# Optimization experiments

Measured on AMD Instinct MI355X. Metric: run time of the kernel, lower is better.

## Reference

```python
import jax, jax.numpy as jnp
import numpy as np

DIM = 512
NUM_HEADS = 8
HEAD_SIZE = 64
INNER = NUM_HEADS * HEAD_SIZE  # 512


def setup_inputs() -> dict:
    key = jax.random.key(0)
    k1, k2, k3, k4, k5 = jax.random.split(key, 5)
    x = jax.random.normal(k1, (2, 4096, DIM), dtype=jnp.float32)
    # Linear params stored as [in, out] for y = x @ W + b (same math as torch Linear)
    w_qkv = jax.random.normal(k2, (DIM, INNER * 3), dtype=jnp.float32) * (1.0 / np.sqrt(DIM))
    b_qkv = jax.random.normal(k3, (INNER * 3,), dtype=jnp.float32) * 0.01
    w_out = jax.random.normal(k4, (INNER, DIM), dtype=jnp.float32) * (1.0 / np.sqrt(INNER))
    b_out = jax.random.normal(k5, (DIM,), dtype=jnp.float32) * 0.01
    return {"x": x, "w_qkv": w_qkv, "b_qkv": b_qkv, "w_out": w_out, "b_out": b_out}


def reference(x, w_qkv, b_qkv, w_out, b_out):
    b, n, _ = x.shape
    qkv = x @ w_qkv + b_qkv                      # [b, n, 3*inner]
    q, k, v = jnp.split(qkv, 3, axis=-1)          # each [b, n, inner]

    def heads(t):  # 'b n (h d) -> b h n d'
        return t.reshape(b, n, NUM_HEADS, HEAD_SIZE).transpose(0, 2, 1, 3)

    q, k, v = heads(q), heads(k), heads(v)
    scores = jnp.einsum('bhnd,bhmd->bhnm', q, k) / jnp.sqrt(jnp.float32(HEAD_SIZE))
    probs = jax.nn.softmax(scores, axis=-1)       # dropout is identity in eval
    out = jnp.einsum('bhnm,bhmd->bhnd', probs, v)
    out = out.transpose(0, 2, 1, 3).reshape(b, n, INNER)  # 'b h n d -> b n (h d)'
    return out @ w_out + b_out
```

## Files before the change

### kernel.cpp

```cpp
#include <hip/hip_runtime.h>

typedef __bf16 bf16;
typedef __bf16 bf16x8 __attribute__((ext_vector_type(8)));
typedef float f32x4 __attribute__((ext_vector_type(4)));
typedef unsigned u32x4 __attribute__((ext_vector_type(4)));

#define MFMA16(a, b, c) __builtin_amdgcn_mfma_f32_16x16x32_bf16((a), (b), (c), 0, 0, 0)

static __device__ __forceinline__ bf16x8 ldg8(const bf16* p) {
  return *(const bf16x8*)p;
}
static __device__ __forceinline__ unsigned cvt_pk_bf16(float lo, float hi) {
  unsigned d;
  asm("v_cvt_pk_bf16_f32 %0, %1, %2" : "=v"(d) : "v"(lo), "v"(hi));
  return d;
}
static __device__ __forceinline__ void pl32_swap(unsigned& a, unsigned& b) {
  asm("v_permlane32_swap_b32 %0, %1" : "+v"(a), "+v"(b));
}
static __device__ __forceinline__ void pl16_swap(unsigned& a, unsigned& b) {
  asm("v_permlane16_swap_b32 %0, %1" : "+v"(a), "+v"(b));
}


__global__ __launch_bounds__(256) void pack_weights(const float* __restrict__ Wqkv,
                                                    const float* __restrict__ Wout,
                                                    bf16* __restrict__ Wp1,
                                                    bf16* __restrict__ Wp2) {
  __shared__ float tile[32 * 129];
  int kc = blockIdx.x, nt = blockIdx.y;
  const float* W;
  bf16* dst;
  int N, ntl;
  if (nt < 12) {
    W = Wqkv; N = 1536; ntl = nt;
    dst = Wp1 + ((size_t)ntl * 16 + kc) * 4096;
  } else {
    W = Wout; N = 512; ntl = nt - 12;
    dst = Wp2 + ((size_t)ntl * 16 + kc) * 4096;
  }
  int row = threadIdx.x >> 3;
  int c0 = (threadIdx.x & 7) * 16;
  const float* src = W + (size_t)(kc * 32 + row) * N + ntl * 128 + c0;
#pragma unroll
  for (int i = 0; i < 4; i++) {
    float4 v = *(const float4*)(src + i * 4);
    tile[row * 129 + c0 + i * 4 + 0] = v.x;
    tile[row * 129 + c0 + i * 4 + 1] = v.y;
    tile[row * 129 + c0 + i * 4 + 2] = v.z;
    tile[row * 129 + c0 + i * 4 + 3] = v.w;
  }
  __syncthreads();
#pragma unroll
  for (int half = 0; half < 2; half++) {
    int U = threadIdx.x + half * 256;
    int kchunk = U >> 7, n = U & 127;
    bf16x8 o;
#pragma unroll
    for (int j = 0; j < 8; j++) o[j] = (bf16)tile[(kchunk * 8 + j) * 129 + n];
    *(bf16x8*)&dst[U * 8] = o;
  }
}

__global__ __launch_bounds__(256, 3) void qkv_gemm(const float* __restrict__ x,
                                                   const bf16* __restrict__ Wp1,
                                                   const float* __restrict__ bqkv,
                                                   bf16* __restrict__ Q,
                                                   bf16* __restrict__ Kh,
                                                   bf16* __restrict__ Vt) {
  int mt = blockIdx.x, nt = blockIdx.y;
  int tid = threadIdx.x;
  int wave = tid >> 6, lane = tid & 63;
  int l16 = lane & 15, quad = lane >> 4;
  int wr = wave >> 1, wc = wave & 1;

  __shared__ __align__(16) bf16 SM[16384];

  int r = tid >> 1, khalf = tid & 1;
  const float* xs = x + (size_t)(mt * 128 + r) * 512 + khalf * 16;
  const bf16* Bt = Wp1 + (size_t)nt * 16 * 4096;
  int lwA0 = ((khalf * 2 + 0) * 128 + r) * 8;
  int lwA1 = ((khalf * 2 + 1) * 128 + r) * 8;

  float4 fa0 = *(const float4*)(xs + 0);
  float4 fa1 = *(const float4*)(xs + 4);
  float4 fa2 = *(const float4*)(xs + 8);
  float4 fa3 = *(const float4*)(xs + 12);
  bf16x8 pb0 = ldg8(Bt + tid * 8), pb1 = ldg8(Bt + 2048 + tid * 8);

  f32x4 acc[4][4] = {};
#pragma unroll 2
  for (int kc = 0; kc < 16; kc++) {
    bf16* A = SM + (kc & 1) * 4096;
    bf16* B = SM + 8192 + (kc & 1) * 4096;
    bf16x8 a0, a1;
    a0[0] = (bf16)fa0.x; a0[1] = (bf16)fa0.y; a0[2] = (bf16)fa0.z; a0[3] = (bf16)fa0.w;
    a0[4] = (bf16)fa1.x; a0[5] = (bf16)fa1.y; a0[6] = (bf16)fa1.z; a0[7] = (bf16)fa1.w;
    a1[0] = (bf16)fa2.x; a1[1] = (bf16)fa2.y; a1[2] = (bf16)fa2.z; a1[3] = (bf16)fa2.w;
    a1[4] = (bf16)fa3.x; a1[5] = (bf16)fa3.y; a1[6] = (bf16)fa3.z; a1[7] = (bf16)fa3.w;
    *(bf16x8*)&A[lwA0] = a0;
    *(bf16x8*)&A[lwA1] = a1;
    *(bf16x8*)&B[tid * 8] = pb0;
    *(bf16x8*)&B[2048 + tid * 8] = pb1;
    __syncthreads();
    if (kc < 15) {
      const float* xn = xs + (kc + 1) * 32;
      fa0 = *(const float4*)(xn + 0);
      fa1 = *(const float4*)(xn + 4);
      fa2 = *(const float4*)(xn + 8);
      fa3 = *(const float4*)(xn + 12);
      const bf16* bn = Bt + (kc + 1) * 4096;
      pb0 = ldg8(bn + tid * 8);
      pb1 = ldg8(bn + 2048 + tid * 8);
    }
    bf16x8 af[4], bfr[4];
#pragma unroll
    for (int fi = 0; fi < 4; fi++)
      af[fi] = *(const bf16x8*)&A[(quad * 128 + wr * 64 + fi * 16 + l16) * 8];
#pragma unroll
    for (int fj = 0; fj < 4; fj++)
      bfr[fj] = *(const bf16x8*)&B[(quad * 128 + wc * 64 + fj * 16 + l16) * 8];
    __builtin_amdgcn_s_setprio(1);
#pragma unroll
    for (int fi = 0; fi < 4; fi++)
#pragma unroll
      for (int fj = 0; fj < 4; fj++)
        acc[fi][fj] = MFMA16(af[fi], bfr[fj], acc[fi][fj]);
    __builtin_amdgcn_s_setprio(0);
  }

  __syncthreads();
  const int TS = 72;
  int b = mt >> 5;

  if (nt < 8) {
    bool isQ = nt < 4;
    bf16* dstb = isQ ? Q : Kh;
    int hb = isQ ? nt * 2 : (nt - 4) * 2;
#pragma unroll
    for (int ph = 0; ph < 2; ph++) {
      if (wc == ph) {
#pragma unroll
        for (int fj = 0; fj < 4; fj++) {
          float bias = bqkv[nt * 128 + wc * 64 + fj * 16 + l16];
#pragma unroll
          for (int fi = 0; fi < 4; fi++)
#pragma unroll
            for (int rr = 0; rr < 4; rr++) {
              float v = acc[fi][fj][rr] + bias;
              if (isQ) v *= 0.18033688f;
              SM[(wr * 64 + fi * 16 + quad * 4 + rr) * TS + fj * 16 + l16] =
                  (bf16)v;
            }
        }
      }
      __syncthreads();
      int bh = b * 8 + hb + ph;
      bf16* dh = dstb + (size_t)bh * 4096 * 64 + (size_t)((mt & 31) * 128) * 64;
#pragma unroll
      for (int i = 0; i < 4; i++) {
        int U = tid + i * 256;
        int mr = U >> 3, oct = U & 7;
        bf16x8 v = ldg8(&SM[mr * TS + oct * 8]);
        *(bf16x8*)&dh[(size_t)mr * 64 + oct * 8] = v;
      }
      __syncthreads();
    }
  } else {
    int h0 = (nt - 8) * 2;
#pragma unroll
    for (int ph = 0; ph < 2; ph++) {
      if (wr == ph) {
#pragma unroll
        for (int fj = 0; fj < 4; fj++) {
          float bias = bqkv[nt * 128 + wc * 64 + fj * 16 + l16];
          int cp = wc * 64 + fj * 16 + l16;
#pragma unroll
          for (int fi = 0; fi < 4; fi++)
#pragma unroll
            for (int rr = 0; rr < 4; rr++)
              SM[cp * TS + fi * 16 + quad * 4 + rr] =
                  (bf16)(acc[fi][fj][rr] + bias);
        }
      }
      __syncthreads();
      int nb = (mt & 31) * 2 + ph;
#pragma unroll
      for (int i = 0; i < 4; i++) {
        int U = tid + i * 256;
        int cp = U >> 3, oct = U & 7;
        int h = h0 + (cp >> 6), d = cp & 63;
        int bh = b * 8 + h;
        bf16x8 v = ldg8(&SM[cp * TS + oct * 8]);
        *(bf16x8*)&Vt[(((size_t)bh * 64 + nb) * 64 + d) * 64 + oct * 8] = v;
      }
      __syncthreads();
    }
  }
}

__global__ __launch_bounds__(256, 4) void flash_partial(const bf16* __restrict__ Q,
                                                        const bf16* __restrict__ K,
                                                        const bf16* __restrict__ Vt,
                                                        bf16* __restrict__ Opart,
                                                        float* __restrict__ Lpart) {
  int strip = blockIdx.x, bh = blockIdx.y, qtr = blockIdx.z;
  int tid = threadIdx.x;
  int wave = tid >> 6, lane = tid & 63;
  int l16 = lane & 15, quad = lane >> 4;

  const bf16* Qh = Q + (size_t)bh * 4096 * 64;
  const bf16* Kg = K + ((size_t)bh * 4096 + qtr * 1024) * 64;
  const bf16* Vg = Vt + (size_t)bh * 64 * 4096 + (size_t)qtr * 1024 * 64;

  __shared__ __align__(16) bf16 Klds[2][4096];
  __shared__ __align__(16) bf16 Vlds[2][4096];

  int qbase = strip * 128 + wave * 32;
  bf16x8 aq[2][2];
#pragma unroll
  for (int mt = 0; mt < 2; mt++) {
    const bf16* qr = Qh + (size_t)(qbase + mt * 16 + l16) * 64;
    aq[mt][0] = ldg8(qr + quad * 8);
    aq[mt][1] = ldg8(qr + 32 + quad * 8);
  }

  bf16x8 ones;
#pragma unroll
  for (int i = 0; i < 8; i++) ones[i] = (bf16)1.0f;

  f32x4 o[2][4] = {};
  f32x4 acc_l[2] = {};

  int e0 = tid * 8, e1 = (256 + tid) * 8;
  int r0 = e0 >> 6, r1 = e1 >> 6;
  int u0 = r0 * 8 + (((e0 & 63) >> 3) ^ (r0 & 7));
  int u1 = r1 * 8 + (((e1 & 63) >> 3) ^ (r1 & 7));

  bf16x8 kp0 = ldg8(Kg + e0), kp1 = ldg8(Kg + e1);
  bf16x8 vp0 = ldg8(Vg + e0), vp1 = ldg8(Vg + e1);

#pragma unroll 2
  for (int t = 0; t < 16; t++) {
    int cur = t & 1;
    bf16* kl = Klds[cur];
    bf16* vl = Vlds[cur];
    *(bf16x8*)&kl[u0 * 8] = kp0;
    *(bf16x8*)&kl[u1 * 8] = kp1;
    *(bf16x8*)&vl[u0 * 8] = vp0;
    *(bf16x8*)&vl[u1 * 8] = vp1;
    __syncthreads();

    if (t < 15) {
      const bf16* kg = Kg + (size_t)(t + 1) * 4096;
      const bf16* vg = Vg + (size_t)(t + 1) * 4096;
      kp0 = ldg8(kg + e0);
      kp1 = ldg8(kg + e1);
      vp0 = ldg8(vg + e0);
      vp1 = ldg8(vg + e1);
    }

#pragma unroll
    for (int h2 = 0; h2 < 2; h2++) {
      f32x4 s[2][2] = {};
      __builtin_amdgcn_s_setprio(1);
#pragma unroll
      for (int c2 = 0; c2 < 2; c2++) {
        int n = h2 * 32 + c2 * 16 + l16;
        bf16x8 k0 = *(const bf16x8*)&kl[(n * 8 + (quad ^ (n & 7))) * 8];
        bf16x8 k1 = *(const bf16x8*)&kl[(n * 8 + ((4 + quad) ^ (n & 7))) * 8];
#pragma unroll
        for (int mt = 0; mt < 2; mt++) {
          s[mt][c2] = MFMA16(k0, aq[mt][0], s[mt][c2]);
          s[mt][c2] = MFMA16(k1, aq[mt][1], s[mt][c2]);
        }
      }
      __builtin_amdgcn_s_setprio(0);

      bf16x8 pa[2];
#pragma unroll
      for (int mt = 0; mt < 2; mt++) {
        unsigned ue[2], wo[2];
#pragma unroll
        for (int c2 = 0; c2 < 2; c2++) {
          float p0 = __builtin_amdgcn_exp2f(s[mt][c2][0]);
          float p1 = __builtin_amdgcn_exp2f(s[mt][c2][1]);
          float p2 = __builtin_amdgcn_exp2f(s[mt][c2][2]);
          float p3 = __builtin_amdgcn_exp2f(s[mt][c2][3]);
          ue[c2] = cvt_pk_bf16(p0, p1);
          wo[c2] = cvt_pk_bf16(p2, p3);
        }
        pl32_swap(ue[0], ue[1]);
        pl16_swap(ue[0], ue[1]);
        pl32_swap(wo[0], wo[1]);
        pl16_swap(wo[0], wo[1]);
        u32x4 pk = {ue[0], wo[0], ue[1], wo[1]};
        pa[mt] = __builtin_bit_cast(bf16x8, pk);
      }

      __builtin_amdgcn_s_setprio(1);
      acc_l[0] = MFMA16(pa[0], ones, acc_l[0]);
      acc_l[1] = MFMA16(pa[1], ones, acc_l[1]);
#pragma unroll
      for (int ct = 0; ct < 4; ct++) {
        int d = ct * 16 + l16;
        bf16x8 bv = *(const bf16x8*)&vl[(d * 8 + ((h2 * 4 + quad) ^ (d & 7))) * 8];
        o[0][ct] = MFMA16(pa[0], bv, o[0][ct]);
        o[1][ct] = MFMA16(pa[1], bv, o[1][ct]);
      }
      __builtin_amdgcn_s_setprio(0);
    }
  }

  size_t ub = ((size_t)qtr * 16 + bh) * 32 + strip;
  bf16* op = Opart + ub * 8192;
#pragma unroll
  for (int mt = 0; mt < 2; mt++) {
#pragma unroll
    for (int ct = 0; ct < 4; ct++)
#pragma unroll
      for (int r = 0; r < 4; r++)
        op[(wave * 32 + mt * 16 + quad * 4 + r) * 64 + ct * 16 + l16] =
            (bf16)o[mt][ct][r];
    if (l16 == 0) {
#pragma unroll
      for (int r = 0; r < 4; r++)
        Lpart[ub * 128 + wave * 32 + mt * 16 + quad * 4 + r] = acc_l[mt][r];
    }
  }
}

__global__ __launch_bounds__(256) void flash_combine(const bf16* __restrict__ Opart,
                                                     const float* __restrict__ Lpart,
                                                     bf16* __restrict__ Ap) {
  int mt = blockIdx.x, kc = blockIdx.y;
  int b = mt >> 5, strip = mt & 31;
  int h = kc >> 1, d0 = (kc & 1) * 32;
  int bh = b * 8 + h;
  size_t u[4];
#pragma unroll
  for (int q = 0; q < 4; q++) u[q] = ((size_t)q * 16 + bh) * 32 + strip;
  bf16* dst = Ap + ((size_t)mt * 16 + kc) * 4096;
#pragma unroll
  for (int hf = 0; hf < 2; hf++) {
    int U = threadIdx.x + hf * 256;
    int kchunk = U >> 7, r = U & 127;
    float acc[8] = {};
    float ls = 0.f;
#pragma unroll
    for (int q = 0; q < 4; q++) {
      bf16x8 ov = ldg8(&Opart[u[q] * 8192 + r * 64 + d0 + kchunk * 8]);
#pragma unroll
      for (int j = 0; j < 8; j++) acc[j] += (float)ov[j];
      ls += Lpart[u[q] * 128 + r];
    }
    float rl = 1.0f / ls;
    bf16x8 o;
#pragma unroll
    for (int j = 0; j < 8; j++) o[j] = (bf16)(acc[j] * rl);
    *(bf16x8*)&dst[U * 8] = o;
  }
}

__global__ __launch_bounds__(256, 3) void out_gemm(const bf16* __restrict__ Ap,
                                                   const bf16* __restrict__ Wp2,
                                                   const float* __restrict__ bout,
                                                   float* __restrict__ Out) {
  int mt = blockIdx.x, nt = blockIdx.y;
  int tid = threadIdx.x;
  int wave = tid >> 6, lane = tid & 63;
  int l16 = lane & 15, quad = lane >> 4;
  int wr = wave >> 1, wc = wave & 1;

  __shared__ __align__(16) bf16 SM[16384];

  const bf16* At = Ap + (size_t)mt * 16 * 4096;
  const bf16* Bt = Wp2 + (size_t)nt * 16 * 4096;
  bf16x8 pa0 = ldg8(At + tid * 8), pa1 = ldg8(At + 2048 + tid * 8);
  bf16x8 pb0 = ldg8(Bt + tid * 8), pb1 = ldg8(Bt + 2048 + tid * 8);

  f32x4 acc[4][4] = {};
#pragma unroll 2
  for (int kc = 0; kc < 16; kc++) {
    bf16* A = SM + (kc & 1) * 4096;
    bf16* B = SM + 8192 + (kc & 1) * 4096;
    *(bf16x8*)&A[tid * 8] = pa0;
    *(bf16x8*)&A[2048 + tid * 8] = pa1;
    *(bf16x8*)&B[tid * 8] = pb0;
    *(bf16x8*)&B[2048 + tid * 8] = pb1;
    __syncthreads();
    if (kc < 15) {
      const bf16* an = At + (kc + 1) * 4096;
      const bf16* bn = Bt + (kc + 1) * 4096;
      pa0 = ldg8(an + tid * 8);
      pa1 = ldg8(an + 2048 + tid * 8);
      pb0 = ldg8(bn + tid * 8);
      pb1 = ldg8(bn + 2048 + tid * 8);
    }
    bf16x8 af[4], bfr[4];
#pragma unroll
    for (int fi = 0; fi < 4; fi++)
      af[fi] = *(const bf16x8*)&A[(quad * 128 + wr * 64 + fi * 16 + l16) * 8];
#pragma unroll
    for (int fj = 0; fj < 4; fj++)
      bfr[fj] = *(const bf16x8*)&B[(quad * 128 + wc * 64 + fj * 16 + l16) * 8];
    __builtin_amdgcn_s_setprio(1);
#pragma unroll
    for (int fi = 0; fi < 4; fi++)
#pragma unroll
      for (int fj = 0; fj < 4; fj++)
        acc[fi][fj] = MFMA16(af[fi], bfr[fj], acc[fi][fj]);
    __builtin_amdgcn_s_setprio(0);
  }

#pragma unroll
  for (int fj = 0; fj < 4; fj++) {
    int c = nt * 128 + wc * 64 + fj * 16 + l16;
    float bias = bout[c];
#pragma unroll
    for (int fi = 0; fi < 4; fi++) {
#pragma unroll
      for (int r = 0; r < 4; r++) {
        int m = mt * 128 + wr * 64 + fi * 16 + quad * 4 + r;
        Out[(size_t)m * 512 + c] = acc[fi][fj][r] + bias;
      }
    }
  }
}

extern "C" void kernel_launch(void* const* d_in, const int* in_sizes, int n_in,
                              void* d_out, int out_size, void* d_ws,
                              size_t ws_size, hipStream_t stream) {
  const float* x = (const float*)d_in[0];
  const float* w_qkv = (const float*)d_in[1];
  const float* b_qkv = (const float*)d_in[2];
  const float* w_out = (const float*)d_in[3];
  const float* b_out = (const float*)d_in[4];
  float* out = (float*)d_out;

  char* ws = (char*)d_ws;
  bf16* Q = (bf16*)(ws + 0);
  bf16* K = (bf16*)(ws + 8388608);
  bf16* Vt = (bf16*)(ws + 16777216);
  bf16* Wp2 = (bf16*)(ws + 25165824);
  bf16* Opart = (bf16*)(ws + 25690112);
  float* Lpart = (float*)(ws + 59244544);
  bf16* Wp1 = (bf16*)(ws + 34078720);
  bf16* Ap = (bf16*)(ws + 0);

  pack_weights<<<dim3(16, 16), 256, 0, stream>>>(w_qkv, w_out, Wp1, Wp2);
  qkv_gemm<<<dim3(64, 12), 256, 0, stream>>>(x, Wp1, b_qkv, Q, K, Vt);
  flash_partial<<<dim3(32, 16, 4), 256, 0, stream>>>(Q, K, Vt, Opart, Lpart);
  flash_combine<<<dim3(64, 16), 256, 0, stream>>>(Opart, Lpart, Ap);
  out_gemm<<<dim3(64, 4), 256, 0, stream>>>(Ap, Wp2, b_out, out);
}
```

Baseline: 197.6 us.

## Halve flash KV split, load GEMM B from global, shrink out_gemm tiles

Flash attention now splits the KV sequence into 2 parts instead of 4. This halves the partial-output traffic and simplifies the combine kernel, but each block runs a longer loop. The QKV GEMM reads B fragments straight from global memory instead of staging them through LDS, and converts A with packed bf16 conversion instructions. out_gemm uses 64-row tiles with global B loads, doubling its grid for better occupancy at the cost of more redundant B reads.

```diff
diff --git a/kernel.cpp b/kernel.cpp
--- a/kernel.cpp
+++ b/kernel.cpp
@@ -74,7 +74,7 @@
   int l16 = lane & 15, quad = lane >> 4;
   int wr = wave >> 1, wc = wave & 1;
 
-  __shared__ __align__(16) bf16 SM[16384];
+  __shared__ __align__(16) bf16 SM[9216];
 
   int r = tid >> 1, khalf = tid & 1;
   const float* xs = x + (size_t)(mt * 128 + r) * 512 + khalf * 16;
@@ -86,22 +86,17 @@
   float4 fa1 = *(const float4*)(xs + 4);
   float4 fa2 = *(const float4*)(xs + 8);
   float4 fa3 = *(const float4*)(xs + 12);
-  bf16x8 pb0 = ldg8(Bt + tid * 8), pb1 = ldg8(Bt + 2048 + tid * 8);
 
   f32x4 acc[4][4] = {};
 #pragma unroll 2
   for (int kc = 0; kc < 16; kc++) {
     bf16* A = SM + (kc & 1) * 4096;
-    bf16* B = SM + 8192 + (kc & 1) * 4096;
-    bf16x8 a0, a1;
-    a0[0] = (bf16)fa0.x; a0[1] = (bf16)fa0.y; a0[2] = (bf16)fa0.z; a0[3] = (bf16)fa0.w;
-    a0[4] = (bf16)fa1.x; a0[5] = (bf16)fa1.y; a0[6] = (bf16)fa1.z; a0[7] = (bf16)fa1.w;
-    a1[0] = (bf16)fa2.x; a1[1] = (bf16)fa2.y; a1[2] = (bf16)fa2.z; a1[3] = (bf16)fa2.w;
-    a1[4] = (bf16)fa3.x; a1[5] = (bf16)fa3.y; a1[6] = (bf16)fa3.z; a1[7] = (bf16)fa3.w;
-    *(bf16x8*)&A[lwA0] = a0;
-    *(bf16x8*)&A[lwA1] = a1;
-    *(bf16x8*)&B[tid * 8] = pb0;
-    *(bf16x8*)&B[2048 + tid * 8] = pb1;
+    u32x4 pk0 = {cvt_pk_bf16(fa0.x, fa0.y), cvt_pk_bf16(fa0.z, fa0.w),
+                 cvt_pk_bf16(fa1.x, fa1.y), cvt_pk_bf16(fa1.z, fa1.w)};
+    u32x4 pk1 = {cvt_pk_bf16(fa2.x, fa2.y), cvt_pk_bf16(fa2.z, fa2.w),
+                 cvt_pk_bf16(fa3.x, fa3.y), cvt_pk_bf16(fa3.z, fa3.w)};
+    *(bf16x8*)&A[lwA0] = __builtin_bit_cast(bf16x8, pk0);
+    *(bf16x8*)&A[lwA1] = __builtin_bit_cast(bf16x8, pk1);
     __syncthreads();
     if (kc < 15) {
       const float* xn = xs + (kc + 1) * 32;
@@ -109,17 +104,15 @@
       fa1 = *(const float4*)(xn + 4);
       fa2 = *(const float4*)(xn + 8);
       fa3 = *(const float4*)(xn + 12);
-      const bf16* bn = Bt + (kc + 1) * 4096;
-      pb0 = ldg8(bn + tid * 8);
-      pb1 = ldg8(bn + 2048 + tid * 8);
     }
     bf16x8 af[4], bfr[4];
 #pragma unroll
     for (int fi = 0; fi < 4; fi++)
       af[fi] = *(const bf16x8*)&A[(quad * 128 + wr * 64 + fi * 16 + l16) * 8];
+    const bf16* Bk = Bt + kc * 4096;
 #pragma unroll
     for (int fj = 0; fj < 4; fj++)
-      bfr[fj] = *(const bf16x8*)&B[(quad * 128 + wc * 64 + fj * 16 + l16) * 8];
+      bfr[fj] = ldg8(Bk + (quad * 128 + wc * 64 + fj * 16 + l16) * 8);
     __builtin_amdgcn_s_setprio(1);
 #pragma unroll
     for (int fi = 0; fi < 4; fi++)
@@ -204,14 +197,14 @@
                                                         const bf16* __restrict__ Vt,
                                                         bf16* __restrict__ Opart,
                                                         float* __restrict__ Lpart) {
-  int strip = blockIdx.x, bh = blockIdx.y, qtr = blockIdx.z;
+  int strip = blockIdx.x, bh = blockIdx.y, half = blockIdx.z;
   int tid = threadIdx.x;
   int wave = tid >> 6, lane = tid & 63;
   int l16 = lane & 15, quad = lane >> 4;
 
   const bf16* Qh = Q + (size_t)bh * 4096 * 64;
-  const bf16* Kg = K + ((size_t)bh * 4096 + qtr * 1024) * 64;
-  const bf16* Vg = Vt + (size_t)bh * 64 * 4096 + (size_t)qtr * 1024 * 64;
+  const bf16* Kg = K + ((size_t)bh * 4096 + half * 2048) * 64;
+  const bf16* Vg = Vt + (size_t)bh * 64 * 4096 + (size_t)half * 2048 * 64;
 
   __shared__ __align__(16) bf16 Klds[2][4096];
   __shared__ __align__(16) bf16 Vlds[2][4096];
@@ -241,7 +234,7 @@
   bf16x8 vp0 = ldg8(Vg + e0), vp1 = ldg8(Vg + e1);
 
 #pragma unroll 2
-  for (int t = 0; t < 16; t++) {
+  for (int t = 0; t < 32; t++) {
     int cur = t & 1;
     bf16* kl = Klds[cur];
     bf16* vl = Vlds[cur];
@@ -251,7 +244,7 @@
     *(bf16x8*)&vl[u1 * 8] = vp1;
     __syncthreads();
 
-    if (t < 15) {
+    if (t < 31) {
       const bf16* kg = Kg + (size_t)(t + 1) * 4096;
       const bf16* vg = Vg + (size_t)(t + 1) * 4096;
       kp0 = ldg8(kg + e0);
@@ -312,7 +305,7 @@
     }
   }
 
-  size_t ub = ((size_t)qtr * 16 + bh) * 32 + strip;
+  size_t ub = ((size_t)half * 16 + bh) * 32 + strip;
   bf16* op = Opart + ub * 8192;
 #pragma unroll
   for (int mt = 0; mt < 2; mt++) {
@@ -337,32 +330,26 @@
   int b = mt >> 5, strip = mt & 31;
   int h = kc >> 1, d0 = (kc & 1) * 32;
   int bh = b * 8 + h;
-  size_t u[4];
-#pragma unroll
-  for (int q = 0; q < 4; q++) u[q] = ((size_t)q * 16 + bh) * 32 + strip;
+  size_t u0 = (size_t)bh * 32 + strip;
+  size_t u1 = ((size_t)16 + bh) * 32 + strip;
   bf16* dst = Ap + ((size_t)mt * 16 + kc) * 4096;
 #pragma unroll
   for (int hf = 0; hf < 2; hf++) {
     int U = threadIdx.x + hf * 256;
     int kchunk = U >> 7, r = U & 127;
-    float acc[8] = {};
-    float ls = 0.f;
-#pragma unroll
-    for (int q = 0; q < 4; q++) {
-      bf16x8 ov = ldg8(&Opart[u[q] * 8192 + r * 64 + d0 + kchunk * 8]);
-#pragma unroll
-      for (int j = 0; j < 8; j++) acc[j] += (float)ov[j];
-      ls += Lpart[u[q] * 128 + r];
-    }
+    bf16x8 o0 = ldg8(&Opart[u0 * 8192 + r * 64 + d0 + kchunk * 8]);
+    bf16x8 o1 = ldg8(&Opart[u1 * 8192 + r * 64 + d0 + kchunk * 8]);
+    float ls = Lpart[u0 * 128 + r] + Lpart[u1 * 128 + r];
     float rl = 1.0f / ls;
-    bf16x8 o;
-#pragma unroll
-    for (int j = 0; j < 8; j++) o[j] = (bf16)(acc[j] * rl);
-    *(bf16x8*)&dst[U * 8] = o;
-  }
-}
-
-__global__ __launch_bounds__(256, 3) void out_gemm(const bf16* __restrict__ Ap,
+    bf16x8 ov;
+#pragma unroll
+    for (int j = 0; j < 8; j++)
+      ov[j] = (bf16)(((float)o0[j] + (float)o1[j]) * rl);
+    *(bf16x8*)&dst[U * 8] = ov;
+  }
+}
+
+__global__ __launch_bounds__(256, 4) void out_gemm(const bf16* __restrict__ Ap,
                                                    const bf16* __restrict__ Wp2,
                                                    const float* __restrict__ bout,
                                                    float* __restrict__ Out) {
@@ -370,58 +357,48 @@
   int tid = threadIdx.x;
   int wave = tid >> 6, lane = tid & 63;
   int l16 = lane & 15, quad = lane >> 4;
-  int wr = wave >> 1, wc = wave & 1;
-
-  __shared__ __align__(16) bf16 SM[16384];
-
-  const bf16* At = Ap + (size_t)mt * 16 * 4096;
+  int mt128 = mt >> 1, mhalf = mt & 1;
+
+  __shared__ __align__(16) bf16 SM[2][2048];
+
+  const bf16* At = Ap + (size_t)mt128 * 16 * 4096;
   const bf16* Bt = Wp2 + (size_t)nt * 16 * 4096;
-  bf16x8 pa0 = ldg8(At + tid * 8), pa1 = ldg8(At + 2048 + tid * 8);
-  bf16x8 pb0 = ldg8(Bt + tid * 8), pb1 = ldg8(Bt + 2048 + tid * 8);
-
-  f32x4 acc[4][4] = {};
+  int guni = (tid >> 6) * 128 + mhalf * 64 + (tid & 63);
+
+  bf16x8 pa = ldg8(At + guni * 8);
+  f32x4 acc[4][2] = {};
 #pragma unroll 2
   for (int kc = 0; kc < 16; kc++) {
-    bf16* A = SM + (kc & 1) * 4096;
-    bf16* B = SM + 8192 + (kc & 1) * 4096;
-    *(bf16x8*)&A[tid * 8] = pa0;
-    *(bf16x8*)&A[2048 + tid * 8] = pa1;
-    *(bf16x8*)&B[tid * 8] = pb0;
-    *(bf16x8*)&B[2048 + tid * 8] = pb1;
+    bf16* A = SM[kc & 1];
+    *(bf16x8*)&A[tid * 8] = pa;
     __syncthreads();
-    if (kc < 15) {
-      const bf16* an = At + (kc + 1) * 4096;
-      const bf16* bn = Bt + (kc + 1) * 4096;
-      pa0 = ldg8(an + tid * 8);
-      pa1 = ldg8(an + 2048 + tid * 8);
-      pb0 = ldg8(bn + tid * 8);
-      pb1 = ldg8(bn + 2048 + tid * 8);
-    }
-    bf16x8 af[4], bfr[4];
+    if (kc < 15) pa = ldg8(At + (kc + 1) * 4096 + guni * 8);
+    bf16x8 af[4], bfr[2];
 #pragma unroll
     for (int fi = 0; fi < 4; fi++)
-      af[fi] = *(const bf16x8*)&A[(quad * 128 + wr * 64 + fi * 16 + l16) * 8];
-#pragma unroll
-    for (int fj = 0; fj < 4; fj++)
-      bfr[fj] = *(const bf16x8*)&B[(quad * 128 + wc * 64 + fj * 16 + l16) * 8];
+      af[fi] = *(const bf16x8*)&A[(quad * 64 + fi * 16 + l16) * 8];
+    const bf16* Bk = Bt + kc * 4096;
+#pragma unroll
+    for (int fj = 0; fj < 2; fj++)
+      bfr[fj] = ldg8(Bk + (quad * 128 + wave * 32 + fj * 16 + l16) * 8);
     __builtin_amdgcn_s_setprio(1);
 #pragma unroll
     for (int fi = 0; fi < 4; fi++)
 #pragma unroll
-      for (int fj = 0; fj < 4; fj++)
+      for (int fj = 0; fj < 2; fj++)
         acc[fi][fj] = MFMA16(af[fi], bfr[fj], acc[fi][fj]);
     __builtin_amdgcn_s_setprio(0);
   }
 
 #pragma unroll
-  for (int fj = 0; fj < 4; fj++) {
-    int c = nt * 128 + wc * 64 + fj * 16 + l16;
+  for (int fj = 0; fj < 2; fj++) {
+    int c = nt * 128 + wave * 32 + fj * 16 + l16;
     float bias = bout[c];
 #pragma unroll
     for (int fi = 0; fi < 4; fi++) {
 #pragma unroll
       for (int r = 0; r < 4; r++) {
-        int m = mt * 128 + wr * 64 + fi * 16 + quad * 4 + r;
+        int m = mt * 64 + fi * 16 + quad * 4 + r;
         Out[(size_t)m * 512 + c] = acc[fi][fj][r] + bias;
       }
     }
@@ -444,13 +421,13 @@
   bf16* Vt = (bf16*)(ws + 16777216);
   bf16* Wp2 = (bf16*)(ws + 25165824);
   bf16* Opart = (bf16*)(ws + 25690112);
-  float* Lpart = (float*)(ws + 59244544);
-  bf16* Wp1 = (bf16*)(ws + 34078720);
+  float* Lpart = (float*)(ws + 42467328);
+  bf16* Wp1 = (bf16*)(ws + 42991616);
   bf16* Ap = (bf16*)(ws + 0);
 
   pack_weights<<<dim3(16, 16), 256, 0, stream>>>(w_qkv, w_out, Wp1, Wp2);
   qkv_gemm<<<dim3(64, 12), 256, 0, stream>>>(x, Wp1, b_qkv, Q, K, Vt);
-  flash_partial<<<dim3(32, 16, 4), 256, 0, stream>>>(Q, K, Vt, Opart, Lpart);
+  flash_partial<<<dim3(32, 16, 2), 256, 0, stream>>>(Q, K, Vt, Opart, Lpart);
   flash_combine<<<dim3(64, 16), 256, 0, stream>>>(Opart, Lpart, Ap);
-  out_gemm<<<dim3(64, 4), 256, 0, stream>>>(Ap, Wp2, b_out, out);
-}
+  out_gemm<<<dim3(128, 4), 256, 0, stream>>>(Ap, Wp2, b_out, out);
+}
```

Measured after the change: 191.2 us. 3.2% less time.
